# Kernel tuning notes

Hardware: AMD Instinct MI355X
Metric: run time of the kernel (lower is better)

## Reference

```python
import jax, jax.numpy as jnp
import numpy as np

N = 4096        # num_queries == gnn_query_dim
C1 = 1001       # classes + 1
D = 4096        # gnn_query_dim
H_MLP = 1024    # mlp_hidden_dim
H = 256         # hidden_dim
O = 256         # output_dim
TOP_K = 32
BN_EPS = 1e-5


def setup_inputs() -> dict:
    key = jax.random.key(0)
    ks = jax.random.split(key, 14)
    def lin(kw, fan_in, shape):
        s = 1.0 / np.sqrt(fan_in)
        return jax.random.uniform(kw, shape, jnp.float32, -s, s)
    return {
        "probs": jax.random.uniform(ks[0], (N, C1), jnp.float32),
        "bbox_coords": jax.random.uniform(ks[1], (N, 4), jnp.float32),
        "query_emb": jax.random.normal(ks[2], (N, D), jnp.float32) * 0.02,
        "node_emb": jax.random.normal(ks[3], (N, D), jnp.float32) * 0.02,
        "mlp_w1": lin(ks[4], D + 4 + C1, (D + 4 + C1, H_MLP)),
        "mlp_b1": lin(ks[5], D + 4 + C1, (H_MLP,)),
        "mlp_w2": lin(ks[6], H_MLP, (H_MLP, N)),
        "mlp_b2": lin(ks[7], H_MLP, (N,)),
        "conv_w1": lin(ks[8], D, (D, H)),
        "conv_b1": lin(ks[9], D, (H,)),
        "conv_w2": lin(ks[10], H, (H, O)),
        "conv_b2": lin(ks[11], H, (O,)),
        "bn_gamma": jnp.ones((H,), jnp.float32),
        "bn_beta": jnp.zeros((H,), jnp.float32),
    }


def reference(probs, bbox_coords, query_emb, node_emb,
              mlp_w1, mlp_b1, mlp_w2, mlp_b2,
              conv_w1, conv_b1, conv_w2, conv_b2,
              bn_gamma, bn_beta):
    # edge-weight MLP -> dense dynamic adjacency logits (N, N)
    ew_in = jnp.concatenate([query_emb, probs, bbox_coords], axis=-1)
    h = jax.nn.relu(ew_in @ mlp_w1 + mlp_b1)
    adj = h @ mlp_w2 + mlp_b2                      # (N, N)

    # top-k neighbors per node (sparse dynamic graph)
    vals, idx = jax.lax.top_k(adj, TOP_K)          # (N, K), (N, K)

    # GCN symmetric normalization from row-degree (sum of top-k weights)
    deg = jnp.sum(vals, axis=-1)                   # (N,)
    dinv = jnp.where(deg > 0, jax.lax.rsqrt(jnp.maximum(deg, 1e-12)), 0.0)
    wn = vals * dinv[:, None] * dinv[idx]          # (N, K)

    def gcn_conv(x, w, b):
        # gather neighbor features, weighted sum, then linear
        msg = jnp.einsum('nk,nkf->nf', wn, x[idx])  # (N, F)
        return msg @ w + b

    out = gcn_conv(node_emb, conv_w1, conv_b1)      # (N, H)
    # BatchNorm1d (batch statistics, training-mode math)
    mean = jnp.mean(out, axis=0)
    var = jnp.var(out, axis=0)
    out = (out - mean) * jax.lax.rsqrt(var + BN_EPS) * bn_gamma + bn_beta
    out = jax.nn.relu(out)
    # dropout is identity in eval mode
    out = gcn_conv(out, conv_w2, conv_b2)           # (N, O)
    return out
```

## Files before the change

kernel.cpp:

```cpp
#include <hip/hip_runtime.h>
#include <cfloat>

#define N_NODES 4096
#define C1_DIM  1001
#define D_DIM   4096
#define HMLP    1024
#define KCAT    (D_DIM + C1_DIM + 4)
#define K1PAD   5120
#define TOPK    32

typedef unsigned short u16;
typedef __bf16 bf16x8 __attribute__((ext_vector_type(8)));
typedef float  f32x4  __attribute__((ext_vector_type(4)));

__device__ __forceinline__ unsigned rne_bits(float x) {
  const unsigned u = __float_as_uint(x);
  return u + 0x7FFFu + ((u >> 16) & 1u);
}

__device__ __forceinline__ void gload16(const void* g, void* l) {
  __builtin_amdgcn_global_load_lds(
      (const __attribute__((address_space(1))) unsigned int*)g,
      (__attribute__((address_space(3))) unsigned int*)l, 16, 0, 0);
}

__global__ __launch_bounds__(256) void split_q(
    const float* __restrict__ in, u16* __restrict__ hi, u16* __restrict__ lo) {
  const size_t idx = ((size_t)blockIdx.x * 256 + threadIdx.x) * 8;
  const int row = (int)(idx >> 12);
  const int col = (int)(idx & 4095);
  const float4 x0 = *(const float4*)(in + idx);
  const float4 x1 = *(const float4*)(in + idx + 4);
  const float xs[8] = {x0.x, x0.y, x0.z, x0.w, x1.x, x1.y, x1.z, x1.w};
  unsigned hw[4], lw[4];
#pragma unroll
  for (int p = 0; p < 4; ++p) {
    const unsigned v0 = rne_bits(xs[2*p]);
    const unsigned v1 = rne_bits(xs[2*p+1]);
    hw[p] = (v1 & 0xFFFF0000u) | (v0 >> 16);
    const float r0 = xs[2*p]   - __uint_as_float(v0 & 0xFFFF0000u);
    const float r1 = xs[2*p+1] - __uint_as_float(v1 & 0xFFFF0000u);
    lw[p] = (rne_bits(r1) & 0xFFFF0000u) | (rne_bits(r0) >> 16);
  }
  const size_t o = (size_t)row * K1PAD + col;
  *(uint4*)(hi + o) = make_uint4(hw[0], hw[1], hw[2], hw[3]);
  *(uint4*)(lo + o) = make_uint4(lw[0], lw[1], lw[2], lw[3]);
}

__global__ __launch_bounds__(256) void tail_split(
    const float* __restrict__ probs, const float* __restrict__ bbox,
    u16* __restrict__ hi, u16* __restrict__ lo) {
  const int i = blockIdx.x * 256 + threadIdx.x;
  const int n = i >> 10, c = i & 1023;
  float v = 0.f;
  if (c < C1_DIM)          v = probs[n * C1_DIM + c];
  else if (c < C1_DIM + 4) v = bbox[n * 4 + (c - C1_DIM)];
  const unsigned vh = rne_bits(v);
  const float r = v - __uint_as_float(vh & 0xFFFF0000u);
  const size_t o = (size_t)n * K1PAD + D_DIM + c;
  hi[o] = (u16)(vh >> 16);
  lo[o] = (u16)(rne_bits(r) >> 16);
}

__global__ __launch_bounds__(256) void transpose_split(
    const float* __restrict__ in, int R, int C, int Rpad,
    u16* __restrict__ out_hi, u16* __restrict__ out_lo) {
  __shared__ float t[64][65];
  const int rb = blockIdx.x * 64;
  const int cb = blockIdx.y * 64;
  const int tid = threadIdx.x;
  const int lr = tid >> 6, lc = tid & 63;
#pragma unroll
  for (int i = 0; i < 16; ++i) {
    const int r = lr + i * 4;
    const int gr = rb + r;
    t[r][lc] = (gr < R) ? in[(size_t)gr * C + cb + lc] : 0.f;
  }
  __syncthreads();
#pragma unroll
  for (int i = 0; i < 16; ++i) {
    const int c = lr + i * 4;
    const float v = t[lc][c];
    const unsigned vh = rne_bits(v);
    const float r = v - __uint_as_float(vh & 0xFFFF0000u);
    const size_t o = (size_t)(cb + c) * Rpad + rb + lc;
    out_hi[o] = (u16)(vh >> 16);
    out_lo[o] = (u16)(rne_bits(r) >> 16);
  }
}


template<bool RELU, bool OUT_SPLIT, bool HASBIAS>
__device__ __forceinline__ void epilogue_64(
    f32x4 (&acc)[4][2], int row0, int col0, int wr0, int wc0, int lane,
    const float* bias, float* Cf, u16* Chi, u16* Clo, int N) {
#pragma unroll
  for (int mi = 0; mi < 4; ++mi)
#pragma unroll
    for (int ni = 0; ni < 2; ++ni) {
      const int gcol = col0 + wc0 + ni * 16 + (lane & 15);
      const float b = HASBIAS ? bias[gcol] : 0.f;
#pragma unroll
      for (int r = 0; r < 4; ++r) {
        const int grow = row0 + wr0 + mi * 16 + (lane >> 4) * 4 + r;
        float v = acc[mi][ni][r] + b;
        if (RELU) v = fmaxf(v, 0.f);
        if (OUT_SPLIT) {
          const unsigned vh = rne_bits(v);
          Chi[(size_t)grow * N + gcol] = (u16)(vh >> 16);
          const float rr = v - __uint_as_float(vh & 0xFFFF0000u);
          Clo[(size_t)grow * N + gcol] = (u16)(rne_bits(rr) >> 16);
        } else {
          Cf[(size_t)grow * N + gcol] = v;
        }
      }
    }
}

template<bool RELU, bool OUT_SPLIT, bool HASBIAS>
__device__ __forceinline__ void gemm_pipe(
    int bx, int by,
    const u16* __restrict__ Ahi, const u16* __restrict__ Alo, int lda,
    const u16* __restrict__ Bthi, const u16* __restrict__ Btlo, int ldb,
    const float* __restrict__ bias,
    float* __restrict__ Cf, u16* __restrict__ Chi, u16* __restrict__ Clo,
    int N, int K, u16* lds) {
  const int tid = threadIdx.x;
  const int lane = tid & 63, wave = tid >> 6;
  const int row0 = by * 128, col0 = bx * 64;
  const int wr0 = (wave >> 1) * 64, wc0 = (wave & 1) * 32;
  const int srow = tid >> 2;
  const int sk   = ((tid & 3) ^ ((tid >> 3) & 3)) * 8;
  const int wu   = (tid & ~63) * 8;

  f32x4 acc[4][2];
#pragma unroll
  for (int mi = 0; mi < 4; ++mi)
#pragma unroll
    for (int ni = 0; ni < 2; ++ni) acc[mi][ni] = (f32x4){0.f, 0.f, 0.f, 0.f};

  auto stage = [&](int buf, int k0) {
    u16* base = lds + buf * 12288;
    gload16(Ahi + (size_t)(row0 + srow) * lda + k0 + sk,      base + wu);
    gload16(Ahi + (size_t)(row0 + 64 + srow) * lda + k0 + sk, base + 2048 + wu);
    gload16(Alo + (size_t)(row0 + srow) * lda + k0 + sk,      base + 4096 + wu);
    gload16(Alo + (size_t)(row0 + 64 + srow) * lda + k0 + sk, base + 6144 + wu);
    gload16(Bthi + (size_t)(col0 + srow) * ldb + k0 + sk, base + 8192 + wu);
    gload16(Btlo + (size_t)(col0 + srow) * ldb + k0 + sk, base + 10240 + wu);
  };
  auto compute = [&](int buf) {
    u16* base = lds + buf * 12288;
    const int ko_swz = ((lane >> 4) ^ ((lane >> 1) & 3)) * 8;
    const int ar = lane & 15;
    bf16x8 ah[4], al[4], bh[2], bl[2];
#pragma unroll
    for (int mi = 0; mi < 4; ++mi) {
      const int r = wr0 + mi * 16 + ar;
      ah[mi] = *(const bf16x8*)&base[r * 32 + ko_swz];
      al[mi] = *(const bf16x8*)&base[4096 + r * 32 + ko_swz];
    }
#pragma unroll
    for (int ni = 0; ni < 2; ++ni) {
      const int c = wc0 + ni * 16 + ar;
      bh[ni] = *(const bf16x8*)&base[8192 + c * 32 + ko_swz];
      bl[ni] = *(const bf16x8*)&base[10240 + c * 32 + ko_swz];
    }
#pragma unroll
    for (int mi = 0; mi < 4; ++mi)
#pragma unroll
      for (int ni = 0; ni < 2; ++ni) {
        acc[mi][ni] = __builtin_amdgcn_mfma_f32_16x16x32_bf16(ah[mi], bh[ni], acc[mi][ni], 0, 0, 0);
        acc[mi][ni] = __builtin_amdgcn_mfma_f32_16x16x32_bf16(ah[mi], bl[ni], acc[mi][ni], 0, 0, 0);
        acc[mi][ni] = __builtin_amdgcn_mfma_f32_16x16x32_bf16(al[mi], bh[ni], acc[mi][ni], 0, 0, 0);
      }
  };

  const int nk = K >> 5;
  stage(0, 0);
  stage(1, 32);
  int cb = 0;
  for (int k = 0; k < nk; ++k) {
    if (k + 2 < nk) {
      int sb = cb + 2; if (sb >= 3) sb -= 3;
      stage(sb, (k + 2) * 32);
      asm volatile("s_waitcnt vmcnt(12)" ::: "memory");
    } else if (k + 1 < nk) {
      asm volatile("s_waitcnt vmcnt(6)" ::: "memory");
    } else {
      asm volatile("s_waitcnt vmcnt(0)" ::: "memory");
    }
    __builtin_amdgcn_s_barrier();
    compute(cb);
    __builtin_amdgcn_s_barrier();
    ++cb; if (cb >= 3) cb -= 3;
  }

  epilogue_64<RELU, OUT_SPLIT, HASBIAS>(acc, row0, col0, wr0, wc0, lane,
                                        bias, Cf, Chi, Clo, N);
}

template<bool RELU, bool OUT_SPLIT, bool HASBIAS>
__device__ __forceinline__ void gemm_a1(
    int bx, int by,
    const float* __restrict__ Aq,
    const u16* __restrict__ Bthi, const u16* __restrict__ Btlo, int ldb,
    const float* __restrict__ bias,
    float* __restrict__ Cf, u16* __restrict__ Chi, u16* __restrict__ Clo,
    int N, int K, u16* lds) {
  const int tid = threadIdx.x;
  const int lane = tid & 63, wave = tid >> 6;
  const int row0 = by * 128, col0 = bx * 64;
  const int wr0 = (wave >> 1) * 64, wc0 = (wave & 1) * 32;
  const int srow = tid >> 2, skof = (tid & 3) * 8;
  const int sk   = ((tid & 3) ^ ((tid >> 3) & 3)) * 8;
  const int wu = (tid & ~63) * 8;

  f32x4 acc[4][2];
#pragma unroll
  for (int mi = 0; mi < 4; ++mi)
#pragma unroll
    for (int ni = 0; ni < 2; ++ni) acc[mi][ni] = (f32x4){0.f, 0.f, 0.f, 0.f};

  auto stageB = [&](int buf, int k0) {
    u16* base = lds + buf * 12288;
    gload16(Bthi + (size_t)(col0 + srow) * ldb + k0 + sk, base + 8192 + wu);
    gload16(Btlo + (size_t)(col0 + srow) * ldb + k0 + sk, base + 10240 + wu);
  };
  auto loadA1 = [&](int k0, float4* x) {
    const int kk = k0 + skof;
#pragma unroll
    for (int j = 0; j < 2; ++j) {
      const int grow = row0 + srow + j * 64;
      const float* src = Aq + (size_t)grow * D_DIM + kk;
      x[j * 2]     = *(const float4*)src;
      x[j * 2 + 1] = *(const float4*)(src + 4);
    }
  };
  auto writeA1 = [&](int buf, const float4* x) {
    u16* base = lds + buf * 12288;
#pragma unroll
    for (int j = 0; j < 2; ++j) {
      const float xs[8] = {x[j*2].x, x[j*2].y, x[j*2].z, x[j*2].w,
                           x[j*2+1].x, x[j*2+1].y, x[j*2+1].z, x[j*2+1].w};
      unsigned hw[4], lw[4];
#pragma unroll
      for (int p = 0; p < 4; ++p) {
        const unsigned v0 = rne_bits(xs[2*p]);
        const unsigned v1 = rne_bits(xs[2*p+1]);
        hw[p] = (v1 & 0xFFFF0000u) | (v0 >> 16);
        const float r0 = xs[2*p]   - __uint_as_float(v0 & 0xFFFF0000u);
        const float r1 = xs[2*p+1] - __uint_as_float(v1 & 0xFFFF0000u);
        lw[p] = (rne_bits(r1) & 0xFFFF0000u) | (rne_bits(r0) >> 16);
      }
      *(uint4*)&base[(srow + j * 64) * 32 + sk] = make_uint4(hw[0], hw[1], hw[2], hw[3]);
      *(uint4*)&base[4096 + (srow + j * 64) * 32 + sk] = make_uint4(lw[0], lw[1], lw[2], lw[3]);
    }
  };
  auto compute = [&](int buf) {
    u16* base = lds + buf * 12288;
    const int ko_swz = ((lane >> 4) ^ ((lane >> 1) & 3)) * 8;
    const int ar = lane & 15;
    bf16x8 ah[4], al[4], bh[2], bl[2];
#pragma unroll
    for (int mi = 0; mi < 4; ++mi) {
      const int r = wr0 + mi * 16 + ar;
      ah[mi] = *(const bf16x8*)&base[r * 32 + ko_swz];
      al[mi] = *(const bf16x8*)&base[4096 + r * 32 + ko_swz];
    }
#pragma unroll
    for (int ni = 0; ni < 2; ++ni) {
      const int c = wc0 + ni * 16 + ar;
      bh[ni] = *(const bf16x8*)&base[8192 + c * 32 + ko_swz];
      bl[ni] = *(const bf16x8*)&base[10240 + c * 32 + ko_swz];
    }
#pragma unroll
    for (int mi = 0; mi < 4; ++mi)
#pragma unroll
      for (int ni = 0; ni < 2; ++ni) {
        acc[mi][ni] = __builtin_amdgcn_mfma_f32_16x16x32_bf16(ah[mi], bh[ni], acc[mi][ni], 0, 0, 0);
        acc[mi][ni] = __builtin_amdgcn_mfma_f32_16x16x32_bf16(ah[mi], bl[ni], acc[mi][ni], 0, 0, 0);
        acc[mi][ni] = __builtin_amdgcn_mfma_f32_16x16x32_bf16(al[mi], bh[ni], acc[mi][ni], 0, 0, 0);
      }
  };

  int cur = 0;
  float4 x[4];
  loadA1(0, x); stageB(0, 0); writeA1(0, x);
  __syncthreads();
  for (int k0 = 0; k0 < K; k0 += 32) {
    const bool nx = (k0 + 32 < K);
    float4 xn[4];
    if (nx) { loadA1(k0 + 32, xn); stageB(cur ^ 1, k0 + 32); }
    compute(cur);
    if (nx) writeA1(cur ^ 1, xn);
    __syncthreads();
    cur ^= 1;
  }

  epilogue_64<RELU, OUT_SPLIT, HASBIAS>(acc, row0, col0, wr0, wc0, lane,
                                        bias, Cf, Chi, Clo, N);
}

__global__ __launch_bounds__(256, 2) void gemm1_kernel(
    const u16* __restrict__ a_hi, const u16* __restrict__ a_lo,
    const u16* __restrict__ w1t_hi, const u16* __restrict__ w1t_lo,
    const float* __restrict__ b1,
    u16* __restrict__ h_hi, u16* __restrict__ h_lo) {
  __shared__ u16 lds[3 * 12288];
  gemm_pipe<true, true, true>(blockIdx.x, blockIdx.y,
      a_hi, a_lo, K1PAD, w1t_hi, w1t_lo, K1PAD, b1,
      nullptr, h_hi, h_lo, HMLP, K1PAD, lds);
}

__global__ __launch_bounds__(256, 2) void fused2_kernel(
    const u16* __restrict__ h_hi, const u16* __restrict__ h_lo,
    const u16* __restrict__ w2t_hi, const u16* __restrict__ w2t_lo,
    const float* __restrict__ b2, float* __restrict__ adj,
    const float* __restrict__ node,
    const u16* __restrict__ w1ct_hi, const u16* __restrict__ w1ct_lo,
    float* __restrict__ Z1) {
  __shared__ u16 lds[3 * 12288];
  const int bid = blockIdx.x;
  if (bid < 128) {
    gemm_a1<false, false, false>(bid & 3, bid >> 2,
        node, w1ct_hi, w1ct_lo, D_DIM, nullptr,
        Z1, nullptr, nullptr, 256, D_DIM, lds);
  } else {
    const int r = bid - 128;
    gemm_pipe<false, false, true>(r & 63, r >> 6,
        h_hi, h_lo, HMLP, w2t_hi, w2t_lo, HMLP, b2,
        adj, nullptr, nullptr, N_NODES, HMLP, lds);
  }
}

__global__ __launch_bounds__(256) void gemm_small(
    const float* __restrict__ A, const float* __restrict__ B,
    float* __restrict__ C, int M, int Ncols, int K) {
  __shared__ float As[16][68];
  __shared__ float Bs[16][68];
  const int tid = threadIdx.x;
  const int row0 = blockIdx.y * 64, col0 = blockIdx.x * 64;
  const int tx = tid & 15, ty = tid >> 4;
  const int arow = tid >> 2, acol = (tid & 3) * 4;
  const int brow = tid >> 4, bcol = (tid & 15) * 4;

  float acc[4][4];
#pragma unroll
  for (int i = 0; i < 4; ++i)
#pragma unroll
    for (int j = 0; j < 4; ++j) acc[i][j] = 0.f;

  for (int k0 = 0; k0 < K; k0 += 16) {
    const float4 a4 = *(const float4*)(A + (size_t)(row0 + arow) * K + k0 + acol);
    const float4 b4 = *(const float4*)(B + (size_t)(k0 + brow) * Ncols + col0 + bcol);
    __syncthreads();
    As[acol + 0][arow] = a4.x; As[acol + 1][arow] = a4.y;
    As[acol + 2][arow] = a4.z; As[acol + 3][arow] = a4.w;
    *(float4*)&Bs[brow][bcol] = b4;
    __syncthreads();
#pragma unroll
    for (int k = 0; k < 16; ++k) {
      float av[4], bw[4];
      *(float4*)&av[0] = *(const float4*)&As[k][ty * 4];
      *(float4*)&bw[0] = *(const float4*)&Bs[k][tx * 4];
#pragma unroll
      for (int i = 0; i < 4; ++i)
#pragma unroll
        for (int j = 0; j < 4; ++j) acc[i][j] += av[i] * bw[j];
    }
  }

#pragma unroll
  for (int i = 0; i < 4; ++i) {
    const int r = row0 + ty * 4 + i;
    float4 v;
    v.x = acc[i][0]; v.y = acc[i][1]; v.z = acc[i][2]; v.w = acc[i][3];
    *(float4*)(C + (size_t)r * Ncols + col0 + tx * 4) = v;
  }
}

__global__ __launch_bounds__(256) void topk_kernel(
    const float* __restrict__ adj, float* __restrict__ vals,
    int* __restrict__ idxo, float* __restrict__ dinv) {
  __shared__ float sv[N_NODES];
  __shared__ float rw[4];
  __shared__ int   iw[4];
  const int n = blockIdx.x, tid = threadIdx.x;
  const int lane = tid & 63, wave = tid >> 6;
  const float4* rowp = (const float4*)(adj + (size_t)n * N_NODES);

  float mv = -FLT_MAX; int mi = 0x7FFFFFFF;
  for (int g = tid; g < N_NODES / 4; g += 256) {
    const float4 v4 = rowp[g];
    *(float4*)&sv[g * 4] = v4;
    if (v4.x > mv) { mv = v4.x; mi = g * 4 + 0; }
    if (v4.y > mv) { mv = v4.y; mi = g * 4 + 1; }
    if (v4.z > mv) { mv = v4.z; mi = g * 4 + 2; }
    if (v4.w > mv) { mv = v4.w; mi = g * 4 + 3; }
  }

  float sum = 0.f;
  for (int it = 0; it < TOPK; ++it) {
    float bv = mv; int bi = mi;
#pragma unroll
    for (int off = 1; off < 64; off <<= 1) {
      const float ov = __shfl_xor(bv, off);
      const int   oi = __shfl_xor(bi, off);
      if (ov > bv || (ov == bv && oi < bi)) { bv = ov; bi = oi; }
    }
    if (lane == 0) { rw[wave] = bv; iw[wave] = bi; }
    __syncthreads();
    bv = rw[0]; bi = iw[0];
#pragma unroll
    for (int w = 1; w < 4; ++w) {
      const float ov = rw[w]; const int oi = iw[w];
      if (ov > bv || (ov == bv && oi < bi)) { bv = ov; bi = oi; }
    }
    if (tid == 0) {
      vals[(size_t)n * TOPK + it] = bv;
      idxo[(size_t)n * TOPK + it] = bi;
    }
    sum += bv;
    if (tid == ((bi >> 2) & 255)) {
      sv[bi] = -FLT_MAX;
      mv = -FLT_MAX; mi = 0x7FFFFFFF;
      for (int g = tid; g < N_NODES / 4; g += 256) {
#pragma unroll
        for (int e = 0; e < 4; ++e) {
          const float v = sv[g * 4 + e];
          if (v > mv) { mv = v; mi = g * 4 + e; }
        }
      }
    }
    __syncthreads();
  }
  if (tid == 0)
    dinv[n] = (sum > 0.f) ? rsqrtf(fmaxf(sum, 1e-12f)) : 0.f;
}

__global__ __launch_bounds__(256) void agg_kernel(
    const float* __restrict__ Z, const float* __restrict__ vals,
    const int* __restrict__ idxo, const float* __restrict__ dinv,
    const float* __restrict__ bias, float* __restrict__ out) {
  const int n = blockIdx.x, f = threadIdx.x;
  const float dn = dinv[n];
  float acc = bias[f];
#pragma unroll
  for (int k = 0; k < TOPK; ++k) {
    const int   j = idxo[n * TOPK + k];
    const float w = vals[n * TOPK + k] * dn * dinv[j];
    acc += w * Z[(size_t)j * 256 + f];
  }
  out[(size_t)n * 256 + f] = acc;
}

__global__ __launch_bounds__(256) void bn_partial(
    const float* __restrict__ x, float* __restrict__ partial) {
  const int b = blockIdx.x, c = threadIdx.x;
  float s = 0.f, s2 = 0.f;
  for (int r = b * 32; r < b * 32 + 32; ++r) {
    const float v = x[(size_t)r * 256 + c];
    s += v; s2 += v * v;
  }
  partial[(size_t)b * 512 + c]       = s;
  partial[(size_t)b * 512 + 256 + c] = s2;
}

__global__ __launch_bounds__(256) void bn_reduce(
    const float* __restrict__ partial, float* __restrict__ colstats) {
  const int j = blockIdx.x, t = threadIdx.x;
  __shared__ float red[128];
  if (t < 128) red[t] = partial[(size_t)t * 512 + j];
  __syncthreads();
  for (int s = 64; s > 0; s >>= 1) {
    if (t < s) red[t] += red[t + s];
    __syncthreads();
  }
  if (t == 0) colstats[j] = red[0];
}

__global__ __launch_bounds__(256) void bn_apply(
    float* __restrict__ x, const float* __restrict__ colstats,
    const float* __restrict__ gamma, const float* __restrict__ beta) {
  const int i = blockIdx.x * 256 + threadIdx.x;
  const int c = i & 255;
  const float mean = colstats[c] * (1.f / 4096.f);
  float var = colstats[256 + c] * (1.f / 4096.f) - mean * mean;
  var = fmaxf(var, 0.f);
  const float v = (x[i] - mean) * rsqrtf(var + 1e-5f) * gamma[c] + beta[c];
  x[i] = fmaxf(v, 0.f);
}

extern "C" void kernel_launch(void* const* d_in, const int* in_sizes, int n_in,
                              void* d_out, int out_size, void* d_ws, size_t ws_size,
                              hipStream_t stream) {
  const float* probs   = (const float*)d_in[0];
  const float* bbox    = (const float*)d_in[1];
  const float* query   = (const float*)d_in[2];
  const float* node    = (const float*)d_in[3];
  const float* mlp_w1  = (const float*)d_in[4];
  const float* mlp_b1  = (const float*)d_in[5];
  const float* mlp_w2  = (const float*)d_in[6];
  const float* mlp_b2  = (const float*)d_in[7];
  const float* conv_w1 = (const float*)d_in[8];
  const float* conv_b1 = (const float*)d_in[9];
  const float* conv_w2 = (const float*)d_in[10];
  const float* conv_b2 = (const float*)d_in[11];
  const float* gamma   = (const float*)d_in[12];
  const float* beta    = (const float*)d_in[13];

  float* ws = (float*)d_ws;
  size_t off = 0;
  float* R1 = ws + off;  off += (size_t)N_NODES * K1PAD;
  u16* a_hi = (u16*)R1;
  u16* a_lo = a_hi + (size_t)N_NODES * K1PAD;
  float* adj = R1;
  float* spare = R1 + (size_t)N_NODES * N_NODES;
  float* Z1   = spare;
  float* vals = spare + (size_t)N_NODES * 256;
  int*   idxo = (int*)(vals + (size_t)N_NODES * TOPK);
  float* dinv = (float*)idxo + (size_t)N_NODES * TOPK;
  float* partial  = dinv + N_NODES;
  float* colstats = partial + 128 * 512;
  float* R2 = ws + off;  off += (size_t)HMLP * K1PAD;
  u16* w1t_hi = (u16*)R2;
  u16* w1t_lo = w1t_hi + (size_t)HMLP * K1PAD;
  u16* w2t_hi = (u16*)R2;
  u16* w2t_lo = w2t_hi + (size_t)N_NODES * HMLP;
  u16* w1ct_hi = (u16*)(R2 + (size_t)N_NODES * HMLP);
  u16* w1ct_lo = w1ct_hi + (size_t)256 * D_DIM;
  float* out1 = R2 + (size_t)N_NODES * HMLP;
  float* R3 = ws + off;  off += (size_t)N_NODES * HMLP;
  u16* h_hi = (u16*)R3;
  u16* h_lo = h_hi + (size_t)N_NODES * HMLP;
  float* Z2 = adj;

  split_q<<<(N_NODES * D_DIM) / (256 * 8), 256, 0, stream>>>(query, a_hi, a_lo);
  tail_split<<<(N_NODES * 1024) / 256, 256, 0, stream>>>(probs, bbox, a_hi, a_lo);
  transpose_split<<<dim3(K1PAD / 64, HMLP / 64), 256, 0, stream>>>(
      mlp_w1, KCAT, HMLP, K1PAD, w1t_hi, w1t_lo);
  gemm1_kernel<<<dim3(HMLP / 64, N_NODES / 128), 256, 0, stream>>>(
      a_hi, a_lo, w1t_hi, w1t_lo, mlp_b1, h_hi, h_lo);
  transpose_split<<<dim3(HMLP / 64, N_NODES / 64), 256, 0, stream>>>(
      mlp_w2, HMLP, N_NODES, HMLP, w2t_hi, w2t_lo);
  transpose_split<<<dim3(D_DIM / 64, 256 / 64), 256, 0, stream>>>(
      conv_w1, D_DIM, 256, D_DIM, w1ct_hi, w1ct_lo);
  fused2_kernel<<<128 + (N_NODES / 64) * (N_NODES / 128), 256, 0, stream>>>(
      h_hi, h_lo, w2t_hi, w2t_lo, mlp_b2, adj, node, w1ct_hi, w1ct_lo, Z1);
  topk_kernel<<<N_NODES, 256, 0, stream>>>(adj, vals, idxo, dinv);
  agg_kernel<<<N_NODES, 256, 0, stream>>>(Z1, vals, idxo, dinv, conv_b1, out1);
  bn_partial<<<128, 256, 0, stream>>>(out1, partial);
  bn_reduce<<<512, 256, 0, stream>>>(partial, colstats);
  bn_apply<<<N_NODES, 256, 0, stream>>>(out1, colstats, gamma, beta);
  gemm_small<<<dim3(256 / 64, N_NODES / 64), 256, 0, stream>>>(
      out1, conv_w2, Z2, N_NODES, 256, 256);
  agg_kernel<<<N_NODES, 256, 0, stream>>>(Z2, vals, idxo, dinv, conv_b2, (float*)d_out);
}
```

Baseline: 608.4 us.

## Use 128x128 double-buffered tile for the adjacency GEMM in fused kernel

```diff
diff --git a/kernel.cpp b/kernel.cpp
--- a/kernel.cpp
+++ b/kernel.cpp
@@ -118,7 +118,7 @@
 }
 
 template<bool RELU, bool OUT_SPLIT, bool HASBIAS>
-__device__ __forceinline__ void gemm_pipe(
+__device__ __forceinline__ void gemm_pipe3(
     int bx, int by,
     const u16* __restrict__ Ahi, const u16* __restrict__ Alo, int lda,
     const u16* __restrict__ Bthi, const u16* __restrict__ Btlo, int ldb,
@@ -197,6 +197,95 @@
 
   epilogue_64<RELU, OUT_SPLIT, HASBIAS>(acc, row0, col0, wr0, wc0, lane,
                                         bias, Cf, Chi, Clo, N);
+}
+
+template<bool HASBIAS>
+__device__ __forceinline__ void gemm_pipe128(
+    int bx, int by,
+    const u16* __restrict__ Ahi, const u16* __restrict__ Alo, int lda,
+    const u16* __restrict__ Bthi, const u16* __restrict__ Btlo, int ldb,
+    const float* __restrict__ bias, float* __restrict__ Cf,
+    int N, int K, u16* lds) {
+  const int tid = threadIdx.x;
+  const int lane = tid & 63, wave = tid >> 6;
+  const int row0 = by * 128, col0 = bx * 128;
+  const int wr0 = (wave >> 1) * 64, wc0 = (wave & 1) * 64;
+  const int srow = tid >> 2;
+  const int sk   = ((tid & 3) ^ ((tid >> 3) & 3)) * 8;
+  const int wu   = (tid & ~63) * 8;
+
+  f32x4 acc[4][4];
+#pragma unroll
+  for (int mi = 0; mi < 4; ++mi)
+#pragma unroll
+    for (int ni = 0; ni < 4; ++ni) acc[mi][ni] = (f32x4){0.f, 0.f, 0.f, 0.f};
+
+  auto stage = [&](int buf, int k0) {
+    u16* base = lds + buf * 16384;
+    gload16(Ahi + (size_t)(row0 + srow) * lda + k0 + sk,      base + wu);
+    gload16(Ahi + (size_t)(row0 + 64 + srow) * lda + k0 + sk, base + 2048 + wu);
+    gload16(Alo + (size_t)(row0 + srow) * lda + k0 + sk,      base + 4096 + wu);
+    gload16(Alo + (size_t)(row0 + 64 + srow) * lda + k0 + sk, base + 6144 + wu);
+    gload16(Bthi + (size_t)(col0 + srow) * ldb + k0 + sk,      base + 8192 + wu);
+    gload16(Bthi + (size_t)(col0 + 64 + srow) * ldb + k0 + sk, base + 10240 + wu);
+    gload16(Btlo + (size_t)(col0 + srow) * ldb + k0 + sk,      base + 12288 + wu);
+    gload16(Btlo + (size_t)(col0 + 64 + srow) * ldb + k0 + sk, base + 14336 + wu);
+  };
+  auto compute = [&](int buf) {
+    u16* base = lds + buf * 16384;
+    const int ko_swz = ((lane >> 4) ^ ((lane >> 1) & 3)) * 8;
+    const int ar = lane & 15;
+    bf16x8 ah[4], al[4], bh[4], bl[4];
+#pragma unroll
+    for (int mi = 0; mi < 4; ++mi) {
+      const int r = wr0 + mi * 16 + ar;
+      ah[mi] = *(const bf16x8*)&base[r * 32 + ko_swz];
+      al[mi] = *(const bf16x8*)&base[4096 + r * 32 + ko_swz];
+    }
+#pragma unroll
+    for (int ni = 0; ni < 4; ++ni) {
+      const int c = wc0 + ni * 16 + ar;
+      bh[ni] = *(const bf16x8*)&base[8192 + c * 32 + ko_swz];
+      bl[ni] = *(const bf16x8*)&base[12288 + c * 32 + ko_swz];
+    }
+#pragma unroll
+    for (int mi = 0; mi < 4; ++mi)
+#pragma unroll
+      for (int ni = 0; ni < 4; ++ni) {
+        acc[mi][ni] = __builtin_amdgcn_mfma_f32_16x16x32_bf16(ah[mi], bh[ni], acc[mi][ni], 0, 0, 0);
+        acc[mi][ni] = __builtin_amdgcn_mfma_f32_16x16x32_bf16(ah[mi], bl[ni], acc[mi][ni], 0, 0, 0);
+        acc[mi][ni] = __builtin_amdgcn_mfma_f32_16x16x32_bf16(al[mi], bh[ni], acc[mi][ni], 0, 0, 0);
+      }
+  };
+
+  const int nk = K >> 5;
+  stage(0, 0);
+  int cur = 0;
+  for (int k = 0; k < nk; ++k) {
+    if (k + 1 < nk) {
+      stage(cur ^ 1, (k + 1) * 32);
+      asm volatile("s_waitcnt vmcnt(8)" ::: "memory");
+    } else {
+      asm volatile("s_waitcnt vmcnt(0)" ::: "memory");
+    }
+    __builtin_amdgcn_s_barrier();
+    compute(cur);
+    __builtin_amdgcn_s_barrier();
+    cur ^= 1;
+  }
+
+#pragma unroll
+  for (int mi = 0; mi < 4; ++mi)
+#pragma unroll
+    for (int ni = 0; ni < 4; ++ni) {
+      const int gcol = col0 + wc0 + ni * 16 + (lane & 15);
+      const float b = HASBIAS ? bias[gcol] : 0.f;
+#pragma unroll
+      for (int r = 0; r < 4; ++r) {
+        const int grow = row0 + wr0 + mi * 16 + (lane >> 4) * 4 + r;
+        Cf[(size_t)grow * N + gcol] = acc[mi][ni][r] + b;
+      }
+    }
 }
 
 template<bool RELU, bool OUT_SPLIT, bool HASBIAS>
@@ -307,7 +396,7 @@
     const float* __restrict__ b1,
     u16* __restrict__ h_hi, u16* __restrict__ h_lo) {
   __shared__ u16 lds[3 * 12288];
-  gemm_pipe<true, true, true>(blockIdx.x, blockIdx.y,
+  gemm_pipe3<true, true, true>(blockIdx.x, blockIdx.y,
       a_hi, a_lo, K1PAD, w1t_hi, w1t_lo, K1PAD, b1,
       nullptr, h_hi, h_lo, HMLP, K1PAD, lds);
 }
@@ -319,7 +408,7 @@
     const float* __restrict__ node,
     const u16* __restrict__ w1ct_hi, const u16* __restrict__ w1ct_lo,
     float* __restrict__ Z1) {
-  __shared__ u16 lds[3 * 12288];
+  __shared__ u16 lds[2 * 16384];
   const int bid = blockIdx.x;
   if (bid < 128) {
     gemm_a1<false, false, false>(bid & 3, bid >> 2,
@@ -327,9 +416,9 @@
         Z1, nullptr, nullptr, 256, D_DIM, lds);
   } else {
     const int r = bid - 128;
-    gemm_pipe<false, false, true>(r & 63, r >> 6,
+    gemm_pipe128<true>(r & 31, r >> 5,
         h_hi, h_lo, HMLP, w2t_hi, w2t_lo, HMLP, b2,
-        adj, nullptr, nullptr, N_NODES, HMLP, lds);
+        adj, N_NODES, HMLP, lds);
   }
 }
 
@@ -545,7 +634,7 @@
       mlp_w2, HMLP, N_NODES, HMLP, w2t_hi, w2t_lo);
   transpose_split<<<dim3(D_DIM / 64, 256 / 64), 256, 0, stream>>>(
       conv_w1, D_DIM, 256, D_DIM, w1ct_hi, w1ct_lo);
-  fused2_kernel<<<128 + (N_NODES / 64) * (N_NODES / 128), 256, 0, stream>>>(
+  fused2_kernel<<<128 + (N_NODES / 128) * (N_NODES / 128), 256, 0, stream>>>(
       h_hi, h_lo, w2t_hi, w2t_lo, mlp_b2, adj, node, w1ct_hi, w1ct_lo, Z1);
   topk_kernel<<<N_NODES, 256, 0, stream>>>(adj, vals, idxo, dinv);
   agg_kernel<<<N_NODES, 256, 0, stream>>>(Z1, vals, idxo, dinv, conv_b1, out1);
```

After: 603.4 us. About the same (-0.8%).
